# Optimization experiments

Hardware: AMD Instinct MI355X
Metric: run time of the kernel (lower is better)

## Reference

```python
import jax, jax.numpy as jnp
import numpy as np

M, N = 512, 768

def setup_inputs() -> dict:
    key = jax.random.key(0)
    k1, _ = jax.random.split(key)
    repr_ = jax.random.normal(k1, (M, N), dtype=jnp.float32)
    GT = jnp.arange(M, dtype=jnp.int64)
    return {"repr": repr_, "GT": GT}

def reference(repr, GT):
    # Reorder features by ground-truth order: r[k] = repr[GT[k]]
    r = repr[GT]                                  # [M, N]
    # All pairwise differences r_i - r_j, clamped at 0 (relu)
    diff = jnp.maximum(r[:, None, :] - r[None, :, :], 0.0)   # [M, M, N]
    sumsq = jnp.sum(diff * diff, axis=-1)          # [M, M]
    # Only pairs with i < j in GT order contribute
    m = r.shape[0]
    mask = jnp.triu(jnp.ones((m, m), dtype=bool), k=1)
    # Guard sqrt at masked (zero) entries for numerical safety
    norms = jnp.sqrt(jnp.where(mask, sumsq, 1.0))
    return jnp.sum(jnp.where(mask, norms, 0.0))
```

## Files before the change

kernel.cpp:

```cpp
#include <hip/hip_runtime.h>

#define MM 512
#define NN 768
#define BI 8
#define BJ 32
#define NC 128
#define SJ 132


__global__ __launch_bounds__(256, 4)
void ClipPairWiseLossAll_kernel(const float* __restrict__ repr,
                                const int* __restrict__ GT,
                                float* __restrict__ out) {
    __shared__ float ldsJ[BJ * SJ];
    __shared__ float ldsI[BI * SJ];
    __shared__ float red[4];

    const int b = blockIdx.x;
    int tj = 0;
    while (2 * (tj + 1) * (tj + 2) <= b) tj++;
    const int ti = b - 2 * tj * (tj + 1);
    const int ibase = ti * BI;
    const int jbase = tj * BJ;

    const int t    = threadIdx.x;
    const int lane = t & 63;
    const int w    = t >> 6;
    const int jl   = lane & 31;
    const int il   = (w << 1) | (lane >> 5);

    const int gi = ibase + il;
    const int gj = jbase + jl;

    const int sg = t & 31;
    const int sr = t >> 5;

    int growJ[4];
#pragma unroll
    for (int it = 0; it < 4; it++) growJ[it] = GT[jbase + sr + (it << 3)];
    const int growI = GT[ibase + sr];

    float acc0 = 0.f, acc1 = 0.f, acc2 = 0.f, acc3 = 0.f;

    for (int c0 = 0; c0 < NN; c0 += NC) {
#pragma unroll
        for (int it = 0; it < 4; it++) {
            const int r = sr + (it << 3);
            const float4 v = *(const float4*)(repr + (size_t)growJ[it] * NN + c0 + (sg << 2));
            *(float4*)(ldsJ + r * SJ + (sg << 2)) = v;
        }
        {
            const float4 v = *(const float4*)(repr + (size_t)growI * NN + c0 + (sg << 2));
            *(float4*)(ldsI + sr * SJ + (sg << 2)) = v;
        }
        __syncthreads();

        const float* rjp = ldsJ + jl * SJ;
        const float* rip = ldsI + il * SJ;
#pragma unroll 8
        for (int g = 0; g < NC / 4; g++) {
            const float4 rj = *(const float4*)(rjp + (g << 2));
            const float4 ri = *(const float4*)(rip + (g << 2));
            const float d0 = fmaxf(ri.x - rj.x, 0.f);
            const float d1 = fmaxf(ri.y - rj.y, 0.f);
            const float d2 = fmaxf(ri.z - rj.z, 0.f);
            const float d3 = fmaxf(ri.w - rj.w, 0.f);
            acc0 = fmaf(d0, d0, acc0);
            acc1 = fmaf(d1, d1, acc1);
            acc2 = fmaf(d2, d2, acc2);
            acc3 = fmaf(d3, d3, acc3);
        }
        __syncthreads();
    }

    float val = (gi < gj) ? sqrtf(acc0 + acc1 + acc2 + acc3) : 0.f;

#pragma unroll
    for (int off = 32; off > 0; off >>= 1)
        val += __shfl_down(val, off, 64);
    if (lane == 0) red[w] = val;
    __syncthreads();
    if (t == 0) {
        atomicAdd(out, red[0] + red[1] + red[2] + red[3]);
    }
}

extern "C" void kernel_launch(void* const* d_in, const int* in_sizes, int n_in,
                              void* d_out, int out_size, void* d_ws, size_t ws_size,
                              hipStream_t stream) {
    const float* repr = (const float*)d_in[0];
    const int*   GT   = (const int*)d_in[1];
    float* out = (float*)d_out;

    hipMemsetAsync(out, 0, sizeof(float) * (size_t)out_size, stream);

    ClipPairWiseLossAll_kernel<<<544, 256, 0, stream>>>(repr, GT, out);
}
```

Baseline: 75.07 us.

## Use 32x32 pair tiles with 2x2 register blocking and deterministic two-stage reduction

Replaces the 8x32 pair tiles with square 32x32 tiles staged together in one LDS buffer. Each thread now computes a 2x2 block of pair accumulators, so every LDS float4 load is reused twice. The per-block atomicAdd and the memset are dropped in favour of per-block partials in workspace plus a second single-block reduce kernel. This cuts LDS traffic per FLOP and launches only 136 blocks, which may underfill the GPU's compute units.

```diff
diff --git a/kernel.cpp b/kernel.cpp
--- a/kernel.cpp
+++ b/kernel.cpp
@@ -2,87 +2,117 @@
 
 #define MM 512
 #define NN 768
-#define BI 8
-#define BJ 32
+#define TT 32
 #define NC 128
 #define SJ 132
+#define NBLK 136
 
-
-__global__ __launch_bounds__(256, 4)
-void ClipPairWiseLossAll_kernel(const float* __restrict__ repr,
-                                const int* __restrict__ GT,
-                                float* __restrict__ out) {
-    __shared__ float ldsJ[BJ * SJ];
-    __shared__ float ldsI[BI * SJ];
+__global__ __launch_bounds__(256, 2)
+void ClipPairWiseLossAll_pairs(const float* __restrict__ repr,
+                               const int* __restrict__ GT,
+                               float* __restrict__ partial) {
+    __shared__ float lds[64 * SJ];
     __shared__ float red[4];
 
     const int b = blockIdx.x;
     int tj = 0;
-    while (2 * (tj + 1) * (tj + 2) <= b) tj++;
-    const int ti = b - 2 * tj * (tj + 1);
-    const int ibase = ti * BI;
-    const int jbase = tj * BJ;
+    while (((tj + 1) * (tj + 2)) >> 1 <= b) tj++;
+    const int ti = b - ((tj * (tj + 1)) >> 1);
+    const int ibase = ti * TT;
+    const int jbase = tj * TT;
 
-    const int t    = threadIdx.x;
-    const int lane = t & 63;
-    const int w    = t >> 6;
-    const int jl   = lane & 31;
-    const int il   = (w << 1) | (lane >> 5);
-
-    const int gi = ibase + il;
-    const int gj = jbase + jl;
+    const int t  = threadIdx.x;
+    const int tx = t & 15;
+    const int ty = t >> 4;
 
     const int sg = t & 31;
     const int sr = t >> 5;
 
-    int growJ[4];
+    int grow[8];
 #pragma unroll
-    for (int it = 0; it < 4; it++) growJ[it] = GT[jbase + sr + (it << 3)];
-    const int growI = GT[ibase + sr];
+    for (int k = 0; k < 8; k++) {
+        const int r = sr + (k << 3);
+        grow[k] = (r < TT) ? GT[ibase + r] : GT[jbase + (r - TT)];
+    }
 
-    float acc0 = 0.f, acc1 = 0.f, acc2 = 0.f, acc3 = 0.f;
+    float4 a00 = {0,0,0,0}, a01 = {0,0,0,0}, a10 = {0,0,0,0}, a11 = {0,0,0,0};
 
+#pragma unroll 1
     for (int c0 = 0; c0 < NN; c0 += NC) {
 #pragma unroll
-        for (int it = 0; it < 4; it++) {
-            const int r = sr + (it << 3);
-            const float4 v = *(const float4*)(repr + (size_t)growJ[it] * NN + c0 + (sg << 2));
-            *(float4*)(ldsJ + r * SJ + (sg << 2)) = v;
-        }
-        {
-            const float4 v = *(const float4*)(repr + (size_t)growI * NN + c0 + (sg << 2));
-            *(float4*)(ldsI + sr * SJ + (sg << 2)) = v;
+        for (int k = 0; k < 8; k++) {
+            const int r = sr + (k << 3);
+            const float4 v = *(const float4*)(repr + (size_t)grow[k] * NN + c0 + (sg << 2));
+            *(float4*)(lds + r * SJ + (sg << 2)) = v;
         }
         __syncthreads();
 
-        const float* rjp = ldsJ + jl * SJ;
-        const float* rip = ldsI + il * SJ;
-#pragma unroll 8
+        const float* ri0 = lds + ty * SJ;
+        const float* ri1 = lds + (ty + 16) * SJ;
+        const float* rj0 = lds + (TT + tx) * SJ;
+        const float* rj1 = lds + (TT + 16 + tx) * SJ;
+
+#pragma unroll 4
         for (int g = 0; g < NC / 4; g++) {
-            const float4 rj = *(const float4*)(rjp + (g << 2));
-            const float4 ri = *(const float4*)(rip + (g << 2));
-            const float d0 = fmaxf(ri.x - rj.x, 0.f);
-            const float d1 = fmaxf(ri.y - rj.y, 0.f);
-            const float d2 = fmaxf(ri.z - rj.z, 0.f);
-            const float d3 = fmaxf(ri.w - rj.w, 0.f);
-            acc0 = fmaf(d0, d0, acc0);
-            acc1 = fmaf(d1, d1, acc1);
-            acc2 = fmaf(d2, d2, acc2);
-            acc3 = fmaf(d3, d3, acc3);
+            const float4 vi0 = *(const float4*)(ri0 + (g << 2));
+            const float4 vi1 = *(const float4*)(ri1 + (g << 2));
+            const float4 vj0 = *(const float4*)(rj0 + (g << 2));
+            const float4 vj1 = *(const float4*)(rj1 + (g << 2));
+
+            float d;
+            d = fmaxf(vi0.x - vj0.x, 0.f); a00.x = fmaf(d, d, a00.x);
+            d = fmaxf(vi0.y - vj0.y, 0.f); a00.y = fmaf(d, d, a00.y);
+            d = fmaxf(vi0.z - vj0.z, 0.f); a00.z = fmaf(d, d, a00.z);
+            d = fmaxf(vi0.w - vj0.w, 0.f); a00.w = fmaf(d, d, a00.w);
+
+            d = fmaxf(vi0.x - vj1.x, 0.f); a01.x = fmaf(d, d, a01.x);
+            d = fmaxf(vi0.y - vj1.y, 0.f); a01.y = fmaf(d, d, a01.y);
+            d = fmaxf(vi0.z - vj1.z, 0.f); a01.z = fmaf(d, d, a01.z);
+            d = fmaxf(vi0.w - vj1.w, 0.f); a01.w = fmaf(d, d, a01.w);
+
+            d = fmaxf(vi1.x - vj0.x, 0.f); a10.x = fmaf(d, d, a10.x);
+            d = fmaxf(vi1.y - vj0.y, 0.f); a10.y = fmaf(d, d, a10.y);
+            d = fmaxf(vi1.z - vj0.z, 0.f); a10.z = fmaf(d, d, a10.z);
+            d = fmaxf(vi1.w - vj0.w, 0.f); a10.w = fmaf(d, d, a10.w);
+
+            d = fmaxf(vi1.x - vj1.x, 0.f); a11.x = fmaf(d, d, a11.x);
+            d = fmaxf(vi1.y - vj1.y, 0.f); a11.y = fmaf(d, d, a11.y);
+            d = fmaxf(vi1.z - vj1.z, 0.f); a11.z = fmaf(d, d, a11.z);
+            d = fmaxf(vi1.w - vj1.w, 0.f); a11.w = fmaf(d, d, a11.w);
         }
         __syncthreads();
     }
 
-    float val = (gi < gj) ? sqrtf(acc0 + acc1 + acc2 + acc3) : 0.f;
+    const int gi0 = ibase + ty, gi1 = ibase + ty + 16;
+    const int gj0 = jbase + tx, gj1 = jbase + tx + 16;
+    float val = 0.f;
+    if (gi0 < gj0) val += sqrtf(a00.x + a00.y + a00.z + a00.w);
+    if (gi0 < gj1) val += sqrtf(a01.x + a01.y + a01.z + a01.w);
+    if (gi1 < gj0) val += sqrtf(a10.x + a10.y + a10.z + a10.w);
+    if (gi1 < gj1) val += sqrtf(a11.x + a11.y + a11.z + a11.w);
 
 #pragma unroll
     for (int off = 32; off > 0; off >>= 1)
         val += __shfl_down(val, off, 64);
+    const int lane = t & 63, w = t >> 6;
     if (lane == 0) red[w] = val;
     __syncthreads();
-    if (t == 0) {
-        atomicAdd(out, red[0] + red[1] + red[2] + red[3]);
-    }
+    if (t == 0) partial[b] = red[0] + red[1] + red[2] + red[3];
+}
+
+__global__ __launch_bounds__(256)
+void ClipPairWiseLossAll_reduce(const float* __restrict__ partial,
+                                float* __restrict__ out) {
+    __shared__ float red[4];
+    const int t = threadIdx.x;
+    float v = (t < NBLK) ? partial[t] : 0.f;
+#pragma unroll
+    for (int off = 32; off > 0; off >>= 1)
+        v += __shfl_down(v, off, 64);
+    const int lane = t & 63, w = t >> 6;
+    if (lane == 0) red[w] = v;
+    __syncthreads();
+    if (t == 0) out[0] = red[0] + red[1] + red[2] + red[3];
 }
 
 extern "C" void kernel_launch(void* const* d_in, const int* in_sizes, int n_in,
@@ -91,8 +121,8 @@
     const float* repr = (const float*)d_in[0];
     const int*   GT   = (const int*)d_in[1];
     float* out = (float*)d_out;
+    float* partial = (float*)d_ws;
 
-    hipMemsetAsync(out, 0, sizeof(float) * (size_t)out_size, stream);
-
-    ClipPairWiseLossAll_kernel<<<544, 256, 0, stream>>>(repr, GT, out);
+    ClipPairWiseLossAll_pairs<<<NBLK, 256, 0, stream>>>(repr, GT, partial);
+    ClipPairWiseLossAll_reduce<<<1, 256, 0, stream>>>(partial, out);
 }
```

Result: slower. 80.07 us (+6.7%).

## Use 64x64 register-blocked tiles with split-K partials and a finish kernel

Applied to the files above, without the earlier changes.

Replaces the 8x32 pair tiles, where each thread owns one pair, with 64x64 triangular tiles in which each thread computes a 4x4 register block. This cuts LDS loads per FMA considerably. The feature dimension is split into 12 chunks spread across blocks, and per-pair partial sums are written to workspace. A second kernel sums the partials, applies sqrt and the upper-triangle mask, and reduces. In exchange it adds a second launch and workspace traffic (about 7 MB written and read), and the diagonal tiles compute redundant pairs.

```diff
diff --git a/kernel.cpp b/kernel.cpp
--- a/kernel.cpp
+++ b/kernel.cpp
@@ -1,88 +1,116 @@
 #include <hip/hip_runtime.h>
+
 
 #define MM 512
 #define NN 768
-#define BI 8
-#define BJ 32
-#define NC 128
-#define SJ 132
-
+#define TT 64
+#define NTILE 36
+#define NSPLIT 12
+#define NC 64
+#define SJ 68
+#define PPT 4096
+#define SLICE (NTILE * PPT)
 
 __global__ __launch_bounds__(256, 4)
-void ClipPairWiseLossAll_kernel(const float* __restrict__ repr,
-                                const int* __restrict__ GT,
-                                float* __restrict__ out) {
-    __shared__ float ldsJ[BJ * SJ];
-    __shared__ float ldsI[BI * SJ];
-    __shared__ float red[4];
+void ClipPairWiseLossAll_partial(const float* __restrict__ repr,
+                                 const int* __restrict__ GT,
+                                 float* __restrict__ ws) {
+    __shared__ float lds[128 * SJ];
 
-    const int b = blockIdx.x;
+    const int b     = blockIdx.x;
+    const int tile  = b % NTILE;
+    const int chunk = b / NTILE;
     int tj = 0;
-    while (2 * (tj + 1) * (tj + 2) <= b) tj++;
-    const int ti = b - 2 * tj * (tj + 1);
-    const int ibase = ti * BI;
-    const int jbase = tj * BJ;
+    while (((tj + 1) * (tj + 2)) >> 1 <= tile) tj++;
+    const int ti = tile - ((tj * (tj + 1)) >> 1);
+    const int ibase = ti * TT;
+    const int jbase = tj * TT;
+    const int c0    = chunk * NC;
 
-    const int t    = threadIdx.x;
-    const int lane = t & 63;
-    const int w    = t >> 6;
-    const int jl   = lane & 31;
-    const int il   = (w << 1) | (lane >> 5);
+    const int t  = threadIdx.x;
+    const int tx = t & 15;
+    const int ty = t >> 4;
 
-    const int gi = ibase + il;
-    const int gj = jbase + jl;
+    const int sg = t & 15;
+    const int sr = t >> 4;
+#pragma unroll
+    for (int k = 0; k < 8; k++) {
+        const int r = sr + (k << 4);
+        const int row = (r < TT) ? GT[ibase + r] : GT[jbase + (r - TT)];
+        const float4 v = *(const float4*)(repr + (size_t)row * NN + c0 + (sg << 2));
+        *(float4*)(lds + r * SJ + (sg << 2)) = v;
+    }
+    __syncthreads();
 
-    const int sg = t & 31;
-    const int sr = t >> 5;
-
-    int growJ[4];
+    float acc[4][4] = {{0.f}};
+#pragma unroll 2
+    for (int g = 0; g < NC / 4; g++) {
+        float4 vi[4], vj[4];
 #pragma unroll
-    for (int it = 0; it < 4; it++) growJ[it] = GT[jbase + sr + (it << 3)];
-    const int growI = GT[ibase + sr];
-
-    float acc0 = 0.f, acc1 = 0.f, acc2 = 0.f, acc3 = 0.f;
-
-    for (int c0 = 0; c0 < NN; c0 += NC) {
+        for (int m = 0; m < 4; m++)
+            vi[m] = *(const float4*)(lds + (ty + (m << 4)) * SJ + (g << 2));
 #pragma unroll
-        for (int it = 0; it < 4; it++) {
-            const int r = sr + (it << 3);
-            const float4 v = *(const float4*)(repr + (size_t)growJ[it] * NN + c0 + (sg << 2));
-            *(float4*)(ldsJ + r * SJ + (sg << 2)) = v;
+        for (int k = 0; k < 4; k++)
+            vj[k] = *(const float4*)(lds + (TT + tx + (k << 4)) * SJ + (g << 2));
+#pragma unroll
+        for (int m = 0; m < 4; m++) {
+#pragma unroll
+            for (int k = 0; k < 4; k++) {
+                float d, a = acc[m][k];
+                d = fmaxf(vi[m].x - vj[k].x, 0.f); a = fmaf(d, d, a);
+                d = fmaxf(vi[m].y - vj[k].y, 0.f); a = fmaf(d, d, a);
+                d = fmaxf(vi[m].z - vj[k].z, 0.f); a = fmaf(d, d, a);
+                d = fmaxf(vi[m].w - vj[k].w, 0.f); a = fmaf(d, d, a);
+                acc[m][k] = a;
+            }
         }
-        {
-            const float4 v = *(const float4*)(repr + (size_t)growI * NN + c0 + (sg << 2));
-            *(float4*)(ldsI + sr * SJ + (sg << 2)) = v;
-        }
-        __syncthreads();
-
-        const float* rjp = ldsJ + jl * SJ;
-        const float* rip = ldsI + il * SJ;
-#pragma unroll 8
-        for (int g = 0; g < NC / 4; g++) {
-            const float4 rj = *(const float4*)(rjp + (g << 2));
-            const float4 ri = *(const float4*)(rip + (g << 2));
-            const float d0 = fmaxf(ri.x - rj.x, 0.f);
-            const float d1 = fmaxf(ri.y - rj.y, 0.f);
-            const float d2 = fmaxf(ri.z - rj.z, 0.f);
-            const float d3 = fmaxf(ri.w - rj.w, 0.f);
-            acc0 = fmaf(d0, d0, acc0);
-            acc1 = fmaf(d1, d1, acc1);
-            acc2 = fmaf(d2, d2, acc2);
-            acc3 = fmaf(d3, d3, acc3);
-        }
-        __syncthreads();
     }
 
-    float val = (gi < gj) ? sqrtf(acc0 + acc1 + acc2 + acc3) : 0.f;
+    float* wp = ws + (size_t)chunk * SLICE + (size_t)tile * PPT;
+#pragma unroll
+    for (int m = 0; m < 4; m++)
+#pragma unroll
+        for (int k = 0; k < 4; k++)
+            wp[(ty + (m << 4)) * TT + (tx + (k << 4))] = acc[m][k];
+}
+
+__global__ __launch_bounds__(256)
+void ClipPairWiseLossAll_finish(const float* __restrict__ ws,
+                                float* __restrict__ out) {
+    __shared__ float red[4];
+    const int t    = threadIdx.x;
+    const int tile = blockIdx.x >> 2;
+    const int q    = blockIdx.x & 3;
+    int tj = 0;
+    while (((tj + 1) * (tj + 2)) >> 1 <= tile) tj++;
+    const int ti = tile - ((tj * (tj + 1)) >> 1);
+
+    const int iy = (q << 4) + (t >> 4);
+    const int jx = (t & 15) << 2;
+
+    const float* p = ws + (size_t)tile * PPT + iy * TT + jx;
+    float4 s = {0.f, 0.f, 0.f, 0.f};
+#pragma unroll
+    for (int c = 0; c < NSPLIT; c++) {
+        const float4 v = *(const float4*)(p + (size_t)c * SLICE);
+        s.x += v.x; s.y += v.y; s.z += v.z; s.w += v.w;
+    }
+
+    const int gi = ti * TT + iy;
+    const int gj = tj * TT + jx;
+    float val = 0.f;
+    if (gi < gj)     val += sqrtf(s.x);
+    if (gi < gj + 1) val += sqrtf(s.y);
+    if (gi < gj + 2) val += sqrtf(s.z);
+    if (gi < gj + 3) val += sqrtf(s.w);
 
 #pragma unroll
     for (int off = 32; off > 0; off >>= 1)
         val += __shfl_down(val, off, 64);
+    const int lane = t & 63, w = t >> 6;
     if (lane == 0) red[w] = val;
     __syncthreads();
-    if (t == 0) {
-        atomicAdd(out, red[0] + red[1] + red[2] + red[3]);
-    }
+    if (t == 0) atomicAdd(out, red[0] + red[1] + red[2] + red[3]);
 }
 
 extern "C" void kernel_launch(void* const* d_in, const int* in_sizes, int n_in,
@@ -91,8 +119,9 @@
     const float* repr = (const float*)d_in[0];
     const int*   GT   = (const int*)d_in[1];
     float* out = (float*)d_out;
+    float* ws  = (float*)d_ws;
 
     hipMemsetAsync(out, 0, sizeof(float) * (size_t)out_size, stream);
-
-    ClipPairWiseLossAll_kernel<<<544, 256, 0, stream>>>(repr, GT, out);
+    ClipPairWiseLossAll_partial<<<NTILE * NSPLIT, 256, 0, stream>>>(repr, GT, ws);
+    ClipPairWiseLossAll_finish<<<NTILE * 4, 256, 0, stream>>>(ws, out);
 }
```

After: 74.77 us. About the same (-0.4%).
